# Optimization experiments

Hardware: AMD Instinct MI355X
Metric: run time of the kernel (lower is better)

## Reference

```python
import jax, jax.numpy as jnp
import numpy as np

N_HEAD = 16
D_MODEL = 1024
D_HEAD = 64
B = 2
S = 2048      # query length
M = 512       # memory length
K = S + M     # key length
L = 2 * K - 1 # relative position table length
SCALE = 1.0 / np.sqrt(D_MODEL)  # NOTE: module scales by 1/sqrt(d_model), not d_head
EPS = 1e-5


def layer_norm(x, gamma, beta):
    mu = jnp.mean(x, axis=-1, keepdims=True)
    var = jnp.mean(jnp.square(x - mu), axis=-1, keepdims=True)
    return (x - mu) * jax.lax.rsqrt(var + EPS) * gamma + beta


def skew(qpos, mem_len):
    # qpos: (B, H, S, 2K-1) -> relative-position scores aligned to keys (B, H, S, K)
    b, h, s, l = qpos.shape
    k_len = (l + 1) // 2
    pad = jnp.full((b, h, s, 1), -jnp.inf, dtype=qpos.dtype)
    rel = jnp.concatenate([qpos, pad], axis=-1)          # (B,H,S,2K)
    rel = rel.reshape(b, h, s * (l + 1))[..., : s * l]    # drop tail, shift rows
    rel = rel.reshape(b, h, s, l)
    start = (k_len - 1) - mem_len
    return rel[..., start : start + k_len]


def setup_inputs() -> dict:
    key = jax.random.key(0)
    ks = jax.random.split(key, 8)
    w_scale = 1.0 / np.sqrt(D_MODEL)
    hidden = jax.random.normal(ks[0], (B, S, D_MODEL), jnp.float32)
    memory = jax.random.normal(ks[1], (B, M, D_MODEL), jnp.float32)
    pos_emb = jax.random.normal(ks[2], (B, L, D_HEAD), jnp.float32)
    Wq = jax.random.normal(ks[3], (D_MODEL, N_HEAD * D_HEAD), jnp.float32) * w_scale
    Wk = jax.random.normal(ks[4], (D_MODEL, N_HEAD * D_HEAD), jnp.float32) * w_scale
    Wv = jax.random.normal(ks[5], (D_MODEL, N_HEAD * D_HEAD), jnp.float32) * w_scale
    Wo = jax.random.normal(ks[6], (N_HEAD * D_HEAD, D_MODEL), jnp.float32) * w_scale
    gamma = jnp.ones((D_MODEL,), jnp.float32)
    beta = jnp.zeros((D_MODEL,), jnp.float32)
    # causal mask with memory: query i may attend keys j <= i + M; True = drop
    i = jnp.arange(S)[:, None]
    j = jnp.arange(K)[None, :]
    mask = j > (i + M)  # (S, K) bool
    return {"hidden": hidden, "pos_emb": pos_emb, "memory": memory,
            "Wq": Wq, "Wk": Wk, "Wv": Wv, "Wo": Wo,
            "gamma": gamma, "beta": beta, "mask": mask}


def reference(hidden, pos_emb, memory, Wq, Wk, Wv, Wo, gamma, beta, mask):
    combined = jnp.concatenate([memory, hidden], axis=1)  # (B, K, D)
    hn = layer_norm(hidden, gamma, beta)                  # pre_lnorm
    cn = layer_norm(combined, gamma, beta)
    q = (hn @ Wq).reshape(B, S, N_HEAD, D_HEAD).transpose(0, 2, 1, 3)  # (B,H,S,Dh)
    k = (cn @ Wk).reshape(B, K, N_HEAD, D_HEAD).transpose(0, 2, 1, 3)  # (B,H,K,Dh)
    v = (cn @ Wv).reshape(B, K, N_HEAD, D_HEAD).transpose(0, 2, 1, 3)  # (B,H,K,Dh)
    scores = jnp.einsum("bhsd,bhkd->bhsk", q, k)           # content term
    qpos = jnp.einsum("bhsd,bld->bhsl", q, pos_emb)        # position term (B,H,S,2K-1)
    scores = (scores + skew(qpos, M)) * SCALE
    scores = jnp.where(mask[None, None], -jnp.inf, scores)
    attn = jax.nn.softmax(scores, axis=-1)
    atten_vec = jnp.einsum("bhsk,bhkd->bshd", attn, v).reshape(B, S, N_HEAD * D_HEAD)
    output = atten_vec @ Wo
    # faithful quirk: residual uses the layer-normed hidden when pre_lnorm=True
    return hn + output
```

## Files before the change

### kernel.cpp

```cpp
#include <hip/hip_runtime.h>

typedef unsigned short u16;
typedef float f32x4 __attribute__((ext_vector_type(4)));
typedef short short8 __attribute__((ext_vector_type(8)));

#define MFMA_BF16(a, b, c) __builtin_amdgcn_mfma_f32_16x16x32_bf16((a), (b), (c), 0, 0, 0)

#define NEG_BIG (-30000.0f)

typedef __attribute__((address_space(1))) const void gas_void;
typedef __attribute__((address_space(3))) void las_void;

__device__ __forceinline__ float bf2f(u16 v) {
  union { unsigned int u; float f; } c; c.u = ((unsigned int)v) << 16; return c.f;
}
__device__ __forceinline__ u16 f2bf(float f) {
  union { float f; unsigned int u; } c; c.f = f;
  return (u16)((c.u + 0x7fffu + ((c.u >> 16) & 1u)) >> 16);
}

__global__ __launch_bounds__(256) void cast_pe_k(const float* __restrict__ src, u16* __restrict__ dst,
                                                 int n4, int* __restrict__ ctr) {
  const int idx = blockIdx.x * 256 + threadIdx.x;
  if (idx == 0) *ctr = 0;
  if (idx >= n4) return;
  const float4 d = *(const float4*)&src[idx * 4];
  ushort4 o;
  o.x = f2bf(d.x); o.y = f2bf(d.y); o.z = f2bf(d.z); o.w = f2bf(d.w);
  *(ushort4*)&dst[idx * 4] = o;
}

__global__ __launch_bounds__(256) void transpose_k(const float* __restrict__ W0, const float* __restrict__ W1,
                                                   const float* __restrict__ W2, const float* __restrict__ W3,
                                                   u16* __restrict__ Wt) {
  __shared__ float t[32][33];
  const float* W = (blockIdx.z == 0) ? W0 : (blockIdx.z == 1) ? W1 : (blockIdx.z == 2) ? W2 : W3;
  u16* dst = Wt + (size_t)blockIdx.z * 1024 * 1024;
  const int tx = threadIdx.x, ty = threadIdx.y;
  const int x0 = blockIdx.x * 32, y0 = blockIdx.y * 32;
#pragma unroll
  for (int i = 0; i < 32; i += 8)
    t[ty + i][tx] = W[(size_t)(y0 + ty + i) * 1024 + x0 + tx];
  __syncthreads();
#pragma unroll
  for (int i = 0; i < 32; i += 8)
    dst[(size_t)(x0 + ty + i) * 1024 + y0 + tx] = f2bf(t[tx][ty + i]);
}

__global__ __launch_bounds__(256) void ln_k(const float* __restrict__ hid, const float* __restrict__ mem,
                                            const float* __restrict__ gam, const float* __restrict__ bet,
                                            u16* __restrict__ cn) {
  const int row = blockIdx.x;
  const int b = (row >= 2560) ? 1 : 0;
  const int r = row - b * 2560;
  const float* src = (r < 512) ? (mem + ((size_t)b * 512 + r) * 1024)
                               : (hid + ((size_t)b * 2048 + (r - 512)) * 1024);
  const int tid = threadIdx.x;
  const float4 d = *(const float4*)&src[tid * 4];
  float x[4] = {d.x, d.y, d.z, d.w};
  float s = x[0] + x[1] + x[2] + x[3];
  float q = x[0]*x[0] + x[1]*x[1] + x[2]*x[2] + x[3]*x[3];
#pragma unroll
  for (int o = 1; o < 64; o <<= 1) { s += __shfl_xor(s, o); q += __shfl_xor(q, o); }
  __shared__ float sb[4], qsb[4];
  const int wave = tid >> 6;
  if ((tid & 63) == 0) { sb[wave] = s; qsb[wave] = q; }
  __syncthreads();
  s = sb[0] + sb[1] + sb[2] + sb[3];
  q = qsb[0] + qsb[1] + qsb[2] + qsb[3];
  const float mu = s * (1.0f / 1024.0f);
  const float var = q * (1.0f / 1024.0f) - mu * mu;
  const float rstd = rsqrtf(fmaxf(var, 0.0f) + 1e-5f);
  u16 o4[4];
#pragma unroll
  for (int i = 0; i < 4; ++i) {
    const int c = tid * 4 + i;
    o4[i] = f2bf((x[i] - mu) * rstd * gam[c] + bet[c]);
  }
  uint2 pk;
  pk.x = (unsigned)o4[0] | ((unsigned)o4[1] << 16);
  pk.y = (unsigned)o4[2] | ((unsigned)o4[3] << 16);
  *(uint2*)&cn[((size_t)b * 2560 + r) * 1024 + tid * 4] = pk;
}

__global__ __launch_bounds__(256, 3) void gemm128_k(const u16* __restrict__ A, const u16* __restrict__ Bt,
                                                    u16* __restrict__ qb, u16* __restrict__ kbo,
                                                    u16* __restrict__ vtb) {
  __shared__ u16 As[128][64];
  __shared__ u16 Bs[128][64];
  const int tid = threadIdx.x;
  const int lane = tid & 63, w = tid >> 6;
  const int quad = lane >> 4, l15 = lane & 15, r7 = l15 & 7;
  const int wr = w >> 1, wc = w & 1;
  const int row0 = blockIdx.y * 128, col0 = blockIdx.x * 128;
  const int rloc = w * 8 + (lane >> 3);
  const int cg = ((lane & 7) ^ ((lane >> 3) & 7)) * 8;
  const u16* ga = A + (size_t)(row0 + rloc) * 1024 + cg;
  const u16* gb = Bt + (size_t)(col0 + rloc) * 1024 + cg;
  f32x4 z = {0.f, 0.f, 0.f, 0.f};
  f32x4 acc[4][4];
#pragma unroll
  for (int m = 0; m < 4; ++m)
#pragma unroll
    for (int n = 0; n < 4; ++n) acc[m][n] = z;
  for (int kt = 0; kt < 16; ++kt) {
    const int k0 = kt * 64;
#pragma unroll
    for (int g2 = 0; g2 < 4; ++g2) {
      __builtin_amdgcn_global_load_lds((gas_void*)(ga + (size_t)g2 * 32 * 1024 + k0),
                                       (las_void*)(&As[g2 * 32 + w * 8][0]), 16, 0, 0);
      __builtin_amdgcn_global_load_lds((gas_void*)(gb + (size_t)g2 * 32 * 1024 + k0),
                                       (las_void*)(&Bs[g2 * 32 + w * 8][0]), 16, 0, 0);
    }
    __syncthreads();
    short8 af0[4], af1[4];
#pragma unroll
    for (int m = 0; m < 4; ++m) {
      const int row = wr * 64 + m * 16 + l15;
      af0[m] = *(const short8*)&As[row][(quad ^ r7) * 8];
      af1[m] = *(const short8*)&As[row][((quad + 4) ^ r7) * 8];
    }
#pragma unroll
    for (int n = 0; n < 4; ++n) {
      const int row = wc * 64 + n * 16 + l15;
      const short8 bf0 = *(const short8*)&Bs[row][(quad ^ r7) * 8];
      const short8 bf1 = *(const short8*)&Bs[row][((quad + 4) ^ r7) * 8];
#pragma unroll
      for (int m = 0; m < 4; ++m) {
        acc[m][n] = MFMA_BF16(af0[m], bf0, acc[m][n]);
        acc[m][n] = MFMA_BF16(af1[m], bf1, acc[m][n]);
      }
    }
    __syncthreads();
  }
  const int nc = col0 >> 10;
#pragma unroll
  for (int m = 0; m < 4; ++m) {
#pragma unroll
    for (int n = 0; n < 4; ++n) {
#pragma unroll
      for (int r = 0; r < 4; ++r) {
        const int R = row0 + wr * 64 + m * 16 + quad * 4 + r;
        const int C = col0 + wc * 64 + n * 16 + l15;
        const float v = acc[m][n][r];
        const int c = C & 1023, h = c >> 6, dh = c & 63;
        const int b = (R >= 2560) ? 1 : 0, kk = R - b * 2560;
        if (nc == 0) {
          if (kk >= 512)
            qb[(((size_t)(b * 16 + h)) * 2048 + (kk - 512)) * 64 + dh] = f2bf(v * 0.03125f);
        } else if (nc == 1) {
          kbo[(((size_t)(b * 16 + h)) * 2560 + kk) * 64 + dh] = f2bf(v);
        } else {
          vtb[(((size_t)(b * 16 + h)) * 64 + dh) * 2560 + kk] = f2bf(v);
        }
      }
    }
  }
}

__global__ __launch_bounds__(256) void gemm_out_k(const u16* __restrict__ A, const u16* __restrict__ Bt,
                                                  float* __restrict__ outf,
                                                  const u16* __restrict__ resid) {
  __shared__ u16 As[2][64][40];
  __shared__ u16 Bs[2][64][40];
  const int tid = threadIdx.x;
  const int lane = tid & 63, wave = tid >> 6;
  const int quad = lane >> 4, l15 = lane & 15;
  const int row0 = blockIdx.y * 64, col0 = blockIdx.x * 64;
  const int sr = tid >> 2, sc8 = (tid & 3) * 8;
  const u16* ga = A + (size_t)(row0 + sr) * 1024 + sc8;
  const u16* gb = Bt + (size_t)(col0 + sr) * 1024 + sc8;
  f32x4 z = {0.f, 0.f, 0.f, 0.f};
  f32x4 acc[4];
#pragma unroll
  for (int i = 0; i < 4; ++i) acc[i] = z;
  *(uint4*)&As[0][sr][sc8] = *(const uint4*)ga;
  *(uint4*)&Bs[0][sr][sc8] = *(const uint4*)gb;
  __syncthreads();
  for (int it = 0; it < 32; ++it) {
    const int cur = it & 1;
    const int kn = (it + 1 < 32) ? (it + 1) * 32 : it * 32;
    const uint4 ua = *(const uint4*)(ga + kn);
    const uint4 ub = *(const uint4*)(gb + kn);
    const short8 af = *(const short8*)&As[cur][16 * wave + l15][quad * 8];
#pragma unroll
    for (int n = 0; n < 4; ++n)
      acc[n] = MFMA_BF16(af, *(const short8*)&Bs[cur][16 * n + l15][quad * 8], acc[n]);
    *(uint4*)&As[cur ^ 1][sr][sc8] = ua;
    *(uint4*)&Bs[cur ^ 1][sr][sc8] = ub;
    __syncthreads();
  }
#pragma unroll
  for (int n = 0; n < 4; ++n) {
#pragma unroll
    for (int r = 0; r < 4; ++r) {
      const int R = row0 + 16 * wave + quad * 4 + r;
      const int C = col0 + 16 * n + l15;
      const size_t rrow = (size_t)(R >> 11) * 2560 + 512 + (R & 2047);
      outf[(size_t)R * 1024 + C] = acc[n][r] + bf2f(resid[rrow * 1024 + C]);
    }
  }
}

__global__ __launch_bounds__(512, 4) void attn_k(const u16* __restrict__ q, const u16* __restrict__ kb,
                                                 const u16* __restrict__ vt, const u16* __restrict__ pe,
                                                 u16* __restrict__ p0, u16* __restrict__ p1,
                                                 float* __restrict__ l0, float* __restrict__ l1,
                                                 int* __restrict__ ctr) {
  __shared__ u16 Kt[2][64][72];
  __shared__ u16 Vt[2][64][72];
  __shared__ u16 Pw[8][16][68];
  volatile int* mailbox = (volatile int*)&Pw[0][0][64];
  const int tid = threadIdx.x, lane = tid & 63, wave = tid >> 6;
  const int quad = lane >> 4, l15 = lane & 15;
  const int sr = tid >> 3, sc8 = (tid & 7) * 8;
  const f32x4 z = {0.f, 0.f, 0.f, 0.f};
  for (;;) {
    if (tid == 0) *mailbox = atomicAdd(ctr, 1);
    __syncthreads();
    const int item = *mailbox;
    if (item >= 1024) return;
    const int qt = 15 - (item >> 6);
    const int bh = (item & 63) >> 1, half = item & 1;
    const int b = bh >> 4, h = bh & 15;
    const int qi0 = qt * 128 + wave * 16;
    const int nh = qt + 5;
    const int t0 = half * nh, t1 = t0 + nh;
    const u16* qrow = q + ((size_t)bh * 2048 + qi0 + l15) * 64 + quad * 8;
    const short8 aq0 = *(const short8*)qrow;
    const short8 aq1 = *(const short8*)(qrow + 32);
    const u16* pp = pe + ((long)b * 5119 - qi0 + 2032 + l15) * 64 + quad * 8 + (size_t)t0 * 4096;
    f32x4 acc[4];
#pragma unroll
    for (int i = 0; i < 4; ++i) acc[i] = z;
    float lrow[4] = {0.f, 0.f, 0.f, 0.f};
    const int jlast = qi0 + 527;
    *(uint4*)&Kt[0][sr][sc8] = *(const uint4*)&kb[((size_t)bh * 2560 + t0 * 64 + sr) * 64 + sc8];
    *(uint4*)&Vt[0][sr][sc8] = *(const uint4*)&vt[((size_t)bh * 64 + sr) * 2560 + t0 * 64 + sc8];
    __syncthreads();
    for (int jt = t0; jt < t1; ++jt) {
      const int j0 = jt * 64;
      const int cur = (jt - t0) & 1;
      const int jn = (jt + 1 < t1) ? (jt + 1) : jt;
      const uint4 ku = *(const uint4*)&kb[((size_t)bh * 2560 + jn * 64 + sr) * 64 + sc8];
      const uint4 vu = *(const uint4*)&vt[((size_t)bh * 64 + sr) * 2560 + jn * 64 + sc8];
      if (j0 <= jlast) {
        short8 pb[5], pb2[5];
#pragma unroll
        for (int g = 0; g < 5; ++g) {
          pb[g]  = *(const short8*)(pp + 1024 * g);
          pb2[g] = *(const short8*)(pp + 1024 * g + 32);
        }
        f32x4 sc[4];
#pragma unroll
        for (int s = 0; s < 4; ++s) {
          sc[s] = MFMA_BF16(aq0, *(const short8*)&Kt[cur][16 * s + l15][quad * 8], z);
          sc[s] = MFMA_BF16(aq1, *(const short8*)&Kt[cur][16 * s + l15][32 + quad * 8], sc[s]);
        }
        f32x4 qp[5];
#pragma unroll
        for (int g = 0; g < 5; ++g) {
          qp[g] = MFMA_BF16(aq0, pb[g], z);
          qp[g] = MFMA_BF16(aq1, pb2[g], qp[g]);
        }
#pragma unroll
        for (int r = 0; r < 4; ++r) {
          const int di = quad * 4 + r;
          const int o = l15 - di + 15;
          const int src = quad * 16 + (o & 15);
          const float g0 = __shfl(qp[0][r], src);
          const float g1 = __shfl(qp[1][r], src);
          const float g2 = __shfl(qp[2][r], src);
          const float g3 = __shfl(qp[3][r], src);
          const float g4 = __shfl(qp[4][r], src);
          const bool lo = (o < 16);
          float s0 = sc[0][r] + (lo ? g0 : g1);
          float s1 = sc[1][r] + (lo ? g1 : g2);
          float s2 = sc[2][r] + (lo ? g2 : g3);
          float s3 = sc[3][r] + (lo ? g3 : g4);
          const int jlim = qi0 + di + 512 - j0 - l15;
          if (0 > jlim)  s0 = NEG_BIG;
          if (16 > jlim) s1 = NEG_BIG;
          if (32 > jlim) s2 = NEG_BIG;
          if (48 > jlim) s3 = NEG_BIG;
          const float p0v = __expf(s0);
          const float p1v = __expf(s1);
          const float p2v = __expf(s2);
          const float p3v = __expf(s3);
          lrow[r] += (p0v + p1v) + (p2v + p3v);
          Pw[wave][di][l15]      = f2bf(p0v);
          Pw[wave][di][16 + l15] = f2bf(p1v);
          Pw[wave][di][32 + l15] = f2bf(p2v);
          Pw[wave][di][48 + l15] = f2bf(p3v);
        }
        asm volatile("s_waitcnt lgkmcnt(0)" ::: "memory");
        const short8 pf0 = *(const short8*)&Pw[wave][l15][quad * 8];
        const short8 pf1 = *(const short8*)&Pw[wave][l15][32 + quad * 8];
#pragma unroll
        for (int n = 0; n < 4; ++n) {
          acc[n] = MFMA_BF16(pf0, *(const short8*)&Vt[cur][16 * n + l15][quad * 8], acc[n]);
          acc[n] = MFMA_BF16(pf1, *(const short8*)&Vt[cur][16 * n + l15][32 + quad * 8], acc[n]);
        }
      }
      *(uint4*)&Kt[cur ^ 1][sr][sc8] = ku;
      *(uint4*)&Vt[cur ^ 1][sr][sc8] = vu;
      __syncthreads();
      pp += 4096;
    }
    u16* od = half ? p1 : p0;
    float* ol = half ? l1 : l0;
#pragma unroll
    for (int r = 0; r < 4; ++r) {
      float lsum = lrow[r];
#pragma unroll
      for (int o = 1; o < 16; o <<= 1) lsum += __shfl_xor(lsum, o);
      const int s = qi0 + quad * 4 + r;
      if (l15 == 0) ol[(size_t)bh * 2048 + s] = lsum;
#pragma unroll
      for (int n = 0; n < 4; ++n) {
        const int c = h * 64 + n * 16 + l15;
        od[((size_t)b * 2048 + s) * 1024 + c] = f2bf(acc[n][r]);
      }
    }
  }
}

__global__ __launch_bounds__(256) void combine_k(u16* __restrict__ av, const u16* __restrict__ p1,
                                                 const float* __restrict__ l0, const float* __restrict__ l1) {
  const int idx = blockIdx.x * 256 + threadIdx.x;
  const int base = idx * 4;
  const int row = base >> 10;
  const int col = base & 1023;
  const int b = row >> 11, s = row & 2047;
  const int h = col >> 6;
  const size_t li = ((size_t)(b * 16 + h)) * 2048 + s;
  const float inv = 1.0f / (l0[li] + l1[li]);
  const ushort4 a0 = *(const ushort4*)&av[(size_t)base];
  const ushort4 a1 = *(const ushort4*)&p1[(size_t)base];
  ushort4 o;
  o.x = f2bf((bf2f(a0.x) + bf2f(a1.x)) * inv);
  o.y = f2bf((bf2f(a0.y) + bf2f(a1.y)) * inv);
  o.z = f2bf((bf2f(a0.z) + bf2f(a1.z)) * inv);
  o.w = f2bf((bf2f(a0.w) + bf2f(a1.w)) * inv);
  *(ushort4*)&av[(size_t)base] = o;
}

extern "C" void kernel_launch(void* const* d_in, const int* in_sizes, int n_in,
                              void* d_out, int out_size, void* d_ws, size_t ws_size,
                              hipStream_t stream) {
  const float* hidden = (const float*)d_in[0];
  const float* pe     = (const float*)d_in[1];
  const float* memv   = (const float*)d_in[2];
  const float* Wq     = (const float*)d_in[3];
  const float* Wk     = (const float*)d_in[4];
  const float* Wv     = (const float*)d_in[5];
  const float* Wo     = (const float*)d_in[6];
  const float* gam    = (const float*)d_in[7];
  const float* bet    = (const float*)d_in[8];

  u16* ws  = (u16*)d_ws;
  u16* cn  = ws;
  u16* qb  = cn  + (size_t)5120 * 1024;
  u16* kb  = qb  + (size_t)4096 * 1024;
  u16* vt  = kb  + (size_t)5120 * 1024;
  u16* av  = vt  + (size_t)5120 * 1024;
  u16* wt  = av  + (size_t)4096 * 1024;
  u16* peb = wt  + (size_t)4 * 1024 * 1024;
  u16* p1  = peb + (size_t)2 * 5119 * 64;
  float* l0 = (float*)(p1 + (size_t)4096 * 1024);
  float* l1 = l0 + (size_t)32 * 2048;
  int* ctr  = (int*)(l1 + (size_t)32 * 2048);

  const int pe_n4 = (2 * 5119 * 64) / 4;
  cast_pe_k<<<(pe_n4 + 255) / 256, 256, 0, stream>>>(pe, peb, pe_n4, ctr);
  ln_k<<<5120, 256, 0, stream>>>(hidden, memv, gam, bet, cn);
  transpose_k<<<dim3(32, 32, 4), dim3(32, 8), 0, stream>>>(Wq, Wk, Wv, Wo, wt);
  gemm128_k<<<dim3(24, 40), 256, 0, stream>>>(cn, wt, qb, kb, vt);
  attn_k<<<768, 512, 0, stream>>>(qb, kb, vt, peb, av, p1, l0, l1, ctr);
  combine_k<<<4096, 256, 0, stream>>>(av, p1, l0, l1);
  gemm_out_k<<<dim3(16, 64), 256, 0, stream>>>(av, wt + (size_t)3 * 1024 * 1024,
                                               (float*)d_out, cn);
}
```

Baseline: 364.8 us.

## Load K/V fragments directly from global memory, drop LDS staging and block barriers

Removes the shared-memory double buffer for K and V tiles and the per-tile __syncthreads; each wave now loads its MFMA operands for K and V straight from global memory (relying on cache). Each wave also trims its own key-tile loop to its causal limit instead of skipping tiles under a block-wide branch. This is meant to cut barrier stalls and LDS traffic and to raise occupancy by freeing LDS, at the cost of redundant global/L2 reads across the 8 waves and less coalesced V loads. An extra barrier after reading the mailbox guards against a race on its reuse.

New measurement: 495.9 us. 35.9% more time.

```diff
diff --git a/kernel.cpp b/kernel.cpp
--- a/kernel.cpp
+++ b/kernel.cpp
@@ -207,18 +207,16 @@
                                                  u16* __restrict__ p0, u16* __restrict__ p1,
                                                  float* __restrict__ l0, float* __restrict__ l1,
                                                  int* __restrict__ ctr) {
-  __shared__ u16 Kt[2][64][72];
-  __shared__ u16 Vt[2][64][72];
   __shared__ u16 Pw[8][16][68];
   volatile int* mailbox = (volatile int*)&Pw[0][0][64];
   const int tid = threadIdx.x, lane = tid & 63, wave = tid >> 6;
   const int quad = lane >> 4, l15 = lane & 15;
-  const int sr = tid >> 3, sc8 = (tid & 7) * 8;
   const f32x4 z = {0.f, 0.f, 0.f, 0.f};
   for (;;) {
     if (tid == 0) *mailbox = atomicAdd(ctr, 1);
     __syncthreads();
     const int item = *mailbox;
+    __syncthreads();
     if (item >= 1024) return;
     const int qt = 15 - (item >> 6);
     const int bh = (item & 63) >> 1, half = item & 1;
@@ -226,85 +224,78 @@
     const int qi0 = qt * 128 + wave * 16;
     const int nh = qt + 5;
     const int t0 = half * nh, t1 = t0 + nh;
+    const int tl = ((qi0 + 527) >> 6) + 1;
+    const int tlw = (t1 < tl) ? t1 : tl;
     const u16* qrow = q + ((size_t)bh * 2048 + qi0 + l15) * 64 + quad * 8;
     const short8 aq0 = *(const short8*)qrow;
     const short8 aq1 = *(const short8*)(qrow + 32);
+    const u16* kbase = kb + (size_t)bh * 2560 * 64 + quad * 8;
+    const u16* vbase = vt + ((size_t)bh * 64 + l15) * 2560 + quad * 8;
     const u16* pp = pe + ((long)b * 5119 - qi0 + 2032 + l15) * 64 + quad * 8 + (size_t)t0 * 4096;
     f32x4 acc[4];
 #pragma unroll
     for (int i = 0; i < 4; ++i) acc[i] = z;
     float lrow[4] = {0.f, 0.f, 0.f, 0.f};
-    const int jlast = qi0 + 527;
-    *(uint4*)&Kt[0][sr][sc8] = *(const uint4*)&kb[((size_t)bh * 2560 + t0 * 64 + sr) * 64 + sc8];
-    *(uint4*)&Vt[0][sr][sc8] = *(const uint4*)&vt[((size_t)bh * 64 + sr) * 2560 + t0 * 64 + sc8];
-    __syncthreads();
-    for (int jt = t0; jt < t1; ++jt) {
+    for (int jt = t0; jt < tlw; ++jt) {
       const int j0 = jt * 64;
-      const int cur = (jt - t0) & 1;
-      const int jn = (jt + 1 < t1) ? (jt + 1) : jt;
-      const uint4 ku = *(const uint4*)&kb[((size_t)bh * 2560 + jn * 64 + sr) * 64 + sc8];
-      const uint4 vu = *(const uint4*)&vt[((size_t)bh * 64 + sr) * 2560 + jn * 64 + sc8];
-      if (j0 <= jlast) {
-        short8 pb[5], pb2[5];
-#pragma unroll
-        for (int g = 0; g < 5; ++g) {
-          pb[g]  = *(const short8*)(pp + 1024 * g);
-          pb2[g] = *(const short8*)(pp + 1024 * g + 32);
-        }
-        f32x4 sc[4];
-#pragma unroll
-        for (int s = 0; s < 4; ++s) {
-          sc[s] = MFMA_BF16(aq0, *(const short8*)&Kt[cur][16 * s + l15][quad * 8], z);
-          sc[s] = MFMA_BF16(aq1, *(const short8*)&Kt[cur][16 * s + l15][32 + quad * 8], sc[s]);
-        }
-        f32x4 qp[5];
-#pragma unroll
-        for (int g = 0; g < 5; ++g) {
-          qp[g] = MFMA_BF16(aq0, pb[g], z);
-          qp[g] = MFMA_BF16(aq1, pb2[g], qp[g]);
-        }
-#pragma unroll
-        for (int r = 0; r < 4; ++r) {
-          const int di = quad * 4 + r;
-          const int o = l15 - di + 15;
-          const int src = quad * 16 + (o & 15);
-          const float g0 = __shfl(qp[0][r], src);
-          const float g1 = __shfl(qp[1][r], src);
-          const float g2 = __shfl(qp[2][r], src);
-          const float g3 = __shfl(qp[3][r], src);
-          const float g4 = __shfl(qp[4][r], src);
-          const bool lo = (o < 16);
-          float s0 = sc[0][r] + (lo ? g0 : g1);
-          float s1 = sc[1][r] + (lo ? g1 : g2);
-          float s2 = sc[2][r] + (lo ? g2 : g3);
-          float s3 = sc[3][r] + (lo ? g3 : g4);
-          const int jlim = qi0 + di + 512 - j0 - l15;
-          if (0 > jlim)  s0 = NEG_BIG;
-          if (16 > jlim) s1 = NEG_BIG;
-          if (32 > jlim) s2 = NEG_BIG;
-          if (48 > jlim) s3 = NEG_BIG;
-          const float p0v = __expf(s0);
-          const float p1v = __expf(s1);
-          const float p2v = __expf(s2);
-          const float p3v = __expf(s3);
-          lrow[r] += (p0v + p1v) + (p2v + p3v);
-          Pw[wave][di][l15]      = f2bf(p0v);
-          Pw[wave][di][16 + l15] = f2bf(p1v);
-          Pw[wave][di][32 + l15] = f2bf(p2v);
-          Pw[wave][di][48 + l15] = f2bf(p3v);
-        }
-        asm volatile("s_waitcnt lgkmcnt(0)" ::: "memory");
-        const short8 pf0 = *(const short8*)&Pw[wave][l15][quad * 8];
-        const short8 pf1 = *(const short8*)&Pw[wave][l15][32 + quad * 8];
-#pragma unroll
-        for (int n = 0; n < 4; ++n) {
-          acc[n] = MFMA_BF16(pf0, *(const short8*)&Vt[cur][16 * n + l15][quad * 8], acc[n]);
-          acc[n] = MFMA_BF16(pf1, *(const short8*)&Vt[cur][16 * n + l15][32 + quad * 8], acc[n]);
-        }
-      }
-      *(uint4*)&Kt[cur ^ 1][sr][sc8] = ku;
-      *(uint4*)&Vt[cur ^ 1][sr][sc8] = vu;
-      __syncthreads();
+      f32x4 sc[4];
+#pragma unroll
+      for (int s = 0; s < 4; ++s) {
+        const u16* kr = kbase + (size_t)(j0 + 16 * s + l15) * 64;
+        sc[s] = MFMA_BF16(aq0, *(const short8*)kr, z);
+        sc[s] = MFMA_BF16(aq1, *(const short8*)(kr + 32), sc[s]);
+      }
+      f32x4 qp[5];
+#pragma unroll
+      for (int g = 0; g < 5; ++g) {
+        qp[g] = MFMA_BF16(aq0, *(const short8*)(pp + 1024 * g), z);
+        qp[g] = MFMA_BF16(aq1, *(const short8*)(pp + 1024 * g + 32), qp[g]);
+      }
+      short8 vf0[4], vf1[4];
+#pragma unroll
+      for (int n = 0; n < 4; ++n) {
+        const u16* vr = vbase + (size_t)(16 * n) * 2560 + j0;
+        vf0[n] = *(const short8*)vr;
+        vf1[n] = *(const short8*)(vr + 32);
+      }
+#pragma unroll
+      for (int r = 0; r < 4; ++r) {
+        const int di = quad * 4 + r;
+        const int o = l15 - di + 15;
+        const int src = quad * 16 + (o & 15);
+        const float g0 = __shfl(qp[0][r], src);
+        const float g1 = __shfl(qp[1][r], src);
+        const float g2 = __shfl(qp[2][r], src);
+        const float g3 = __shfl(qp[3][r], src);
+        const float g4 = __shfl(qp[4][r], src);
+        const bool lo = (o < 16);
+        float s0 = sc[0][r] + (lo ? g0 : g1);
+        float s1 = sc[1][r] + (lo ? g1 : g2);
+        float s2 = sc[2][r] + (lo ? g2 : g3);
+        float s3 = sc[3][r] + (lo ? g3 : g4);
+        const int jlim = qi0 + di + 512 - j0 - l15;
+        if (0 > jlim)  s0 = NEG_BIG;
+        if (16 > jlim) s1 = NEG_BIG;
+        if (32 > jlim) s2 = NEG_BIG;
+        if (48 > jlim) s3 = NEG_BIG;
+        const float p0v = __expf(s0);
+        const float p1v = __expf(s1);
+        const float p2v = __expf(s2);
+        const float p3v = __expf(s3);
+        lrow[r] += (p0v + p1v) + (p2v + p3v);
+        Pw[wave][di][l15]      = f2bf(p0v);
+        Pw[wave][di][16 + l15] = f2bf(p1v);
+        Pw[wave][di][32 + l15] = f2bf(p2v);
+        Pw[wave][di][48 + l15] = f2bf(p3v);
+      }
+      asm volatile("s_waitcnt lgkmcnt(0)" ::: "memory");
+      const short8 pf0 = *(const short8*)&Pw[wave][l15][quad * 8];
+      const short8 pf1 = *(const short8*)&Pw[wave][l15][32 + quad * 8];
+#pragma unroll
+      for (int n = 0; n < 4; ++n) {
+        acc[n] = MFMA_BF16(pf0, vf0[n], acc[n]);
+        acc[n] = MFMA_BF16(pf1, vf1[n], acc[n]);
+      }
       pp += 4096;
     }
     u16* od = half ? p1 : p0;
```
